# Kernel optimization log

Measured on AMD Instinct MI355X. Metric: run time of the kernel, lower is better.

The kernel has to match this reference:

```python
import jax, jax.numpy as jnp
import numpy as np

N, C, T, V = 64, 256, 120, 25
H, HD = 8, 32
DIM = H * HD  # 256, equals dim
K = 5        # number of joint groups
MAX_HOP = 5  # rpe rows = hops.max()+1


def conv1x1(w, x):
    # 1x1 Conv2d over [N, C, T, V]: pure channel mixing
    return jnp.einsum('oc,nctv->notv', w, x)


def setup_inputs() -> dict:
    key = jax.random.key(0)
    ks = jax.random.split(key, 10)
    s = 0.02
    return {
        'x': jax.random.normal(ks[0], (N, C, T, V), jnp.float32),
        'joint_label': jax.random.uniform(ks[1], (V, K), jnp.float32),
        'hops': jax.random.randint(ks[2], (V, V), 0, MAX_HOP, dtype=jnp.int32),
        'norm1_w': jnp.ones((C,), jnp.float32),
        'norm1_b': jnp.zeros((C,), jnp.float32),
        'q_w': jax.random.normal(ks[3], (DIM, C), jnp.float32) * s,
        'kv_w': jax.random.normal(ks[4], (2 * DIM, C), jnp.float32) * s,
        'proj_w': jax.random.normal(ks[5], (DIM, DIM), jnp.float32) * s,
        'proj_b': jnp.zeros((DIM,), jnp.float32),
        'rpe': jax.random.normal(ks[6], (MAX_HOP, DIM), jnp.float32) * s,
        'w1': jax.random.normal(ks[7], (H, HD), jnp.float32) * s,
        'outer': jnp.broadcast_to(jnp.eye(V, dtype=jnp.float32), (H, V, V)).copy(),
        'alpha': jnp.array([0.5], jnp.float32),
        'pe_w': jax.random.normal(ks[8], (DIM, C), jnp.float32) * s,
    }


def reference(x, joint_label, hops, norm1_w, norm1_b, q_w, kv_w,
              proj_w, proj_b, rpe, w1, outer, alpha, pe_w):
    n, c, t, v = x.shape
    h, hd = w1.shape
    dim = h * hd

    # ---- group embedding e (use_group, use_learned_partition == 'none') ----
    jl = joint_label  # [V, K]
    z = jnp.einsum('nctv,vk->nctk', x, jl / jl.sum(0, keepdims=True))
    z = jnp.einsum('dc,nctk->ndtk', pe_w, z)          # pe_proj (1x1 conv, no bias)
    e = jnp.einsum('ndtk,vk->ndtv', z, jl)            # z @ joint_label.T

    # ---- norm1: LayerNorm over channel dim ----
    mu = x.mean(axis=1, keepdims=True)
    var = x.var(axis=1, keepdims=True)
    xn = (x - mu) / jnp.sqrt(var + 1e-5)
    xn = xn * norm1_w[None, :, None, None] + norm1_b[None, :, None, None]

    # ---- q, k, v: 1x1 convs, reshape to [N, T, H, V, HD] ----
    def to_heads(y):
        return y.reshape(n, h, hd, t, v).transpose(0, 3, 1, 4, 2)

    q = to_heads(conv1x1(q_w, xn))
    k = to_heads(conv1x1(kv_w[:dim], xn))
    vv = to_heads(conv1x1(kv_w[dim:], xn))

    # ---- attention scores + biases ----
    attn = jnp.einsum('bthnc,bthmc->bthnm', q, k)
    # hop relative-position bias
    k_r = rpe[hops].reshape(v, v, h, hd)
    attn = attn + jnp.einsum('bthnc,nmhc->bthnm', q, k_r)
    # group embedding bias
    e_k = to_heads(e)
    attn = attn + jnp.einsum('bthnc,bthmc->bthnm', q, e_k)
    # group bias (broadcast over query dim)
    attn = attn + jnp.einsum('hc,bthmc->bthm', w1, e_k)[:, :, :, None, :]

    scale = hd ** (-0.5)
    attn = jax.nn.softmax(attn * scale, axis=-1)

    # ---- outer-blended attention @ v ----
    mix = alpha[0] * attn + outer[None, None]          # [N,T,H,V,V]
    o = jnp.einsum('bthnm,bthmc->bthnc', mix, vv)      # [N,T,H,V,HD]

    # back to [N, DIM, T, V]
    o = o.transpose(0, 1, 2, 4, 3).reshape(n, t, dim, v).transpose(0, 2, 1, 3)
    o = conv1x1(proj_w, o) + proj_b[None, :, None, None]

    # residual (dim_in == dim => plain skip)
    return x + o
```

## Files before the change

kernel.cpp:

```cpp
#include <hip/hip_runtime.h>


#define N_ 64
#define C_ 256
#define T_ 120
#define V_ 25
#define H_ 8
#define HD_ 32
#define K_ 5
#define TV_ 3000
#define CTV_ 768000

typedef unsigned short u16;
typedef __bf16 bf16x8 __attribute__((ext_vector_type(8)));
typedef float f32x4 __attribute__((ext_vector_type(4)));
typedef u16 u16x4 __attribute__((ext_vector_type(4)));

#define MFMA(a, b, c) __builtin_amdgcn_mfma_f32_16x16x32_bf16(a, b, c, 0, 0, 0)

__device__ __forceinline__ u16 bhi(float f) {
    union { float f; unsigned u; } c; c.f = f; return (u16)(c.u >> 16);
}
__device__ __forceinline__ float bhif(float f) {
    union { float f; unsigned u; } c; c.f = f; c.u &= 0xFFFF0000u; return c.f;
}

#define OFF_XT 0
#define XT_S 268
#define OFF_Z 6700
#define OFF_QB 7980
#define OFF_KB 15148
#define OFF_VB 22316
#define OFF_AT 29516
#define AT_S 27
#define OFF_QR 34916
#define OFF_BIAS 35916
#define OFF_MU 36116
#define OFF_RS 36141
#define OFF_INV 36166
#define OFF_JL 36171
#define OFF_W1 36296
#define OFF_HOPS 36552
#define SMEM_N 37177
#define OFF_PS OFF_VB
#define OFF_PSS (OFF_VB + 256)
#define OFF_Z2 (OFF_QB + 5120)
#define UZTH (OFF_QB * 2)
#define UZTL (OFF_QB * 2 + 4224)

#define WS_Q 0
#define WS_PE 393216
#define WS_PJ 524288

__global__ __launch_bounds__(256) void wprep(
    const float* __restrict__ qw, const float* __restrict__ kvw,
    const float* __restrict__ pew, const float* __restrict__ pjw,
    u16* __restrict__ ws)
{
    int fid = blockIdx.x * 256 + threadIdx.x;
    int seg, f;
    if (fid < 24576)      { seg = 0; f = fid; }
    else if (fid < 32768) { seg = 1; f = fid - 24576; }
    else                  { seg = 2; f = fid - 32768; }
    int mt = f >> 9, rem = f & 511, kt = rem >> 6, l = rem & 63;
    int row = mt * 16 + (l & 15);
    int k0 = kt * 32 + (l >> 4) * 8;
    const float* sp;
    u16* dp;
    if (seg == 0) {
        sp = (row < 256) ? (qw + row * 256 + k0) : (kvw + (row - 256) * 256 + k0);
        dp = ws + WS_Q + f * 16;
    } else if (seg == 1) {
        sp = pew + row * 256 + k0;
        dp = ws + WS_PE + f * 16;
    } else {
        sp = pjw + row * 256 + k0;
        dp = ws + WS_PJ + f * 16;
    }
    float4 a = *(const float4*)sp;
    float4 b = *(const float4*)(sp + 4);
    float w8[8] = {a.x, a.y, a.z, a.w, b.x, b.y, b.z, b.w};
    #pragma unroll
    for (int j = 0; j < 8; ++j) {
        float w = w8[j];
        dp[j] = bhi(w);
        dp[8 + j] = bhi(w - bhif(w));
    }
}

__global__ __launch_bounds__(512, 2) void fused_sttr(
    const float* __restrict__ x, const float* __restrict__ jl,
    const int* __restrict__ hops, const float* __restrict__ n1w,
    const float* __restrict__ n1b, const float* __restrict__ rpe,
    const float* __restrict__ pjb, const float* __restrict__ w1,
    const float* __restrict__ outer, const float* __restrict__ alpha,
    const u16* __restrict__ ws, float* __restrict__ out)
{
    __shared__ float sm[SMEM_N];
    u16* smu = reinterpret_cast<u16*>(sm);
    int* hopsS = (int*)(sm + OFF_HOPS);
    const int tid = threadIdx.x;
    const int bid = blockIdx.x;
    const int n = bid / T_;
    const int t = bid - n * T_;
    const int xbase = n * CTV_ + t * V_;
    const u16* wsq = ws + WS_Q;
    const u16* wspe = ws + WS_PE;
    const u16* wspj = ws + WS_PJ;
    const int wv = tid >> 6, ln = tid & 63;
    const int col = ln & 15, kg = ln >> 4;

    for (int i = tid; i < V_ * K_; i += 512) sm[OFF_JL + i] = jl[i];
    for (int i = tid; i < V_ * V_; i += 512) hopsS[i] = hops[i];
    for (int i = tid; i < H_ * HD_; i += 512) sm[OFF_W1 + i] = w1[i];
    for (int i = tid; i < C_ * V_; i += 512) {
        int c = i / V_, v = i - c * V_;
        sm[OFF_XT + v * XT_S + c] = x[xbase + c * TV_ + v];
    }
    __syncthreads();

    if (tid < K_) {
        float s = 0.f;
        for (int v = 0; v < V_; ++v) s += sm[OFF_JL + v * K_ + tid];
        sm[OFF_INV + tid] = 1.0f / s;
    } else if (tid >= 256 && tid < 456) {
        int i = tid - 256;
        int v = i % V_, p = i / V_;
        const float* row = &sm[OFF_XT + v * XT_S + p * 32];
        float s = 0.f, ss = 0.f;
        #pragma unroll
        for (int j = 0; j < 32; ++j) { float xx = row[j]; s += xx; ss += xx * xx; }
        sm[OFF_PS + p * 32 + v] = s;
        sm[OFF_PSS + p * 32 + v] = ss;
    }
    __syncthreads();

    if (tid < C_) {
        float a0 = 0, a1 = 0, a2 = 0, a3 = 0, a4 = 0;
        #pragma unroll
        for (int v = 0; v < V_; ++v) {
            float xv = sm[OFF_XT + v * XT_S + tid];
            const float* j5 = &sm[OFF_JL + v * K_];
            a0 += xv * j5[0]; a1 += xv * j5[1]; a2 += xv * j5[2];
            a3 += xv * j5[3]; a4 += xv * j5[4];
        }
        float* zr = &sm[OFF_Z + tid * K_];
        zr[0] = a0 * sm[OFF_INV + 0]; zr[1] = a1 * sm[OFF_INV + 1];
        zr[2] = a2 * sm[OFF_INV + 2]; zr[3] = a3 * sm[OFF_INV + 3];
        zr[4] = a4 * sm[OFF_INV + 4];
    } else if (tid < C_ + V_) {
        int v = tid - C_;
        float s = 0.f, ss = 0.f;
        #pragma unroll
        for (int p = 0; p < 8; ++p) { s += sm[OFF_PS + p * 32 + v]; ss += sm[OFF_PSS + p * 32 + v]; }
        float mu = s * (1.0f / 256.0f);
        float var = ss * (1.0f / 256.0f) - mu * mu;
        sm[OFF_MU + v] = mu;
        sm[OFF_RS + v] = rsqrtf(var + 1e-5f);
    }
    __syncthreads();

    float xr[32];
    {
        if (tid < 200) {
            int v = tid >> 3, cb = tid & 7, c0 = cb * 32;
            float mu = sm[OFF_MU + v], rs = sm[OFF_RS + v];
            #pragma unroll
            for (int j = 0; j < 32; ++j) {
                int c = c0 + j;
                xr[j] = (sm[OFF_XT + v * XT_S + c] - mu) * rs * n1w[c] + n1b[c];
            }
        } else if (tid >= 256) {
            int c = tid - 256;
            #pragma unroll
            for (int nn = 0; nn < K_; ++nn) {
                float f = sm[OFF_Z + c * K_ + nn];
                smu[UZTH + nn * 264 + c] = bhi(f);
                smu[UZTL + nn * 264 + c] = bhi(f - bhif(f));
            }
        }
    }
    __syncthreads();
    if (tid < 200) {
        int v = tid >> 3, cb = tid & 7, c0 = cb * 32;
        #pragma unroll
        for (int jb = 0; jb < 8; ++jb) {
            u16x4 hv, lv;
            #pragma unroll
            for (int j = 0; j < 4; ++j) {
                float f = xr[jb * 4 + j];
                hv[j] = bhi(f);
                lv[j] = bhi(f - bhif(f));
            }
            *(u16x4*)&smu[v * 536 + c0 + jb * 4] = hv;
            *(u16x4*)&smu[v * 536 + 256 + c0 + jb * 4] = lv;
        }
    }
    __syncthreads();

    {
        f32x4 zacc[2];
        #pragma unroll
        for (int i = 0; i < 2; ++i)
            #pragma unroll
            for (int r = 0; r < 4; ++r) zacc[i][r] = 0.f;
        for (int kt = 0; kt < 8; ++kt) {
            int bo = kt * 32 + kg * 8;
            bf16x8 zbh = *reinterpret_cast<const bf16x8*>(&smu[UZTH + col * 264 + bo]);
            bf16x8 zbl = *reinterpret_cast<const bf16x8*>(&smu[UZTL + col * 264 + bo]);
            #pragma unroll
            for (int i = 0; i < 2; ++i) {
                const u16* ap = wspe + (((wv * 2 + i) * 8 + kt) * 64 + ln) * 16;
                bf16x8 ah = *reinterpret_cast<const bf16x8*>(ap);
                bf16x8 al = *reinterpret_cast<const bf16x8*>(ap + 8);
                zacc[i] = MFMA(ah, zbh, zacc[i]);
                zacc[i] = MFMA(ah, zbl, zacc[i]);
                zacc[i] = MFMA(al, zbh, zacc[i]);
            }
        }
        if (col < K_) {
            #pragma unroll
            for (int i = 0; i < 2; ++i)
                #pragma unroll
                for (int r = 0; r < 4; ++r)
                    sm[OFF_Z2 + ((wv * 2 + i) * 16 + kg * 4 + r) * 8 + col] = zacc[i][r];
        }
    }
    __syncthreads();

    if (tid < C_) {
        float z0 = sm[OFF_Z2 + tid * 8 + 0], z1 = sm[OFF_Z2 + tid * 8 + 1];
        float z2_ = sm[OFF_Z2 + tid * 8 + 2], z3 = sm[OFF_Z2 + tid * 8 + 3];
        float z4 = sm[OFF_Z2 + tid * 8 + 4];
        float* kb = &sm[OFF_KB + tid * 28];
        #pragma unroll
        for (int v = 0; v < V_; ++v) {
            const float* j5 = &sm[OFF_JL + v * K_];
            kb[v] = z0 * j5[0] + z1 * j5[1] + z2_ * j5[2] + z3 * j5[3] + z4 * j5[4];
        }
    }
    __syncthreads();

    {
        f32x4 acc[6][2];
        #pragma unroll
        for (int i = 0; i < 6; ++i)
            #pragma unroll
            for (int nt = 0; nt < 2; ++nt)
                #pragma unroll
                for (int r = 0; r < 4; ++r) acc[i][nt][r] = 0.f;
        for (int kt = 0; kt < 8; ++kt) {
            int bo = kt * 32 + kg * 8;
            bf16x8 bh0 = *reinterpret_cast<const bf16x8*>(&smu[col * 536 + bo]);
            bf16x8 bl0 = *reinterpret_cast<const bf16x8*>(&smu[col * 536 + 256 + bo]);
            bf16x8 bh1 = *reinterpret_cast<const bf16x8*>(&smu[(col + 16) * 536 + bo]);
            bf16x8 bl1 = *reinterpret_cast<const bf16x8*>(&smu[(col + 16) * 536 + 256 + bo]);
            #pragma unroll
            for (int i = 0; i < 6; ++i) {
                const u16* ap = wsq + (((wv * 6 + i) * 8 + kt) * 64 + ln) * 16;
                bf16x8 ah = *reinterpret_cast<const bf16x8*>(ap);
                bf16x8 al = *reinterpret_cast<const bf16x8*>(ap + 8);
                acc[i][0] = MFMA(ah, bh0, acc[i][0]);
                acc[i][0] = MFMA(ah, bl0, acc[i][0]);
                acc[i][0] = MFMA(al, bh0, acc[i][0]);
                acc[i][1] = MFMA(ah, bh1, acc[i][1]);
                acc[i][1] = MFMA(ah, bl1, acc[i][1]);
                acc[i][1] = MFMA(al, bh1, acc[i][1]);
            }
        }
        if (tid < H_ * V_) {
            int h = tid / V_, m = tid - h * V_;
            float s = 0.f;
            #pragma unroll
            for (int c = 0; c < HD_; ++c)
                s += sm[OFF_W1 + h * HD_ + c] * sm[OFF_KB + (h * HD_ + c) * 28 + m];
            sm[OFF_BIAS + h * V_ + m] = s;
        }
        __syncthreads();
        #pragma unroll
        for (int i = 0; i < 6; ++i) {
            #pragma unroll
            for (int nt = 0; nt < 2; ++nt) {
                int v = nt * 16 + col;
                if (v < V_) {
                    #pragma unroll
                    for (int r = 0; r < 4; ++r) {
                        int row = (wv * 6 + i) * 16 + kg * 4 + r;
                        float val = acc[i][nt][r];
                        if (row < 256) sm[OFF_QB + row * 28 + v] = val;
                        else if (row < 512) sm[OFF_KB + (row - 256) * 28 + v] += val;
                        else {
                            int d = row - 512;
                            sm[OFF_VB + ((d >> 5) * V_ + v) * 36 + (d & 31)] = val;
                        }
                    }
                }
            }
        }
    }
    __syncthreads();

    for (int i = tid; i < H_ * V_ * K_; i += 512) {
        int h = i / (V_ * K_);
        int rem = i - h * (V_ * K_);
        int nq = rem / K_, hop = rem - nq * K_;
        const float* rp = rpe + hop * 256 + h * HD_;
        float s = 0.f;
        #pragma unroll
        for (int c = 0; c < HD_; ++c)
            s += sm[OFF_QB + (h * HD_ + c) * 28 + nq] * rp[c];
        sm[OFF_QR + (h * V_ + nq) * K_ + hop] = s;
    }
    __syncthreads();

    if (tid < 392) {
        int h = tid / 49;
        int r = tid - h * 49;
        int qg = r / 7, mg = r - qg * 7;
        int q0 = qg * 4, m0 = mg * 4;
        float acc[4][4];
        #pragma unroll
        for (int i = 0; i < 4; ++i)
            #pragma unroll
            for (int j = 0; j < 4; ++j) acc[i][j] = 0.f;
        for (int c = 0; c < HD_; ++c) {
            float4 q4 = *(const float4*)&sm[OFF_QB + (h * HD_ + c) * 28 + q0];
            float4 k4 = *(const float4*)&sm[OFF_KB + (h * HD_ + c) * 28 + m0];
            float qa[4] = {q4.x, q4.y, q4.z, q4.w};
            float ka[4] = {k4.x, k4.y, k4.z, k4.w};
            #pragma unroll
            for (int i = 0; i < 4; ++i)
                #pragma unroll
                for (int j = 0; j < 4; ++j) acc[i][j] += qa[i] * ka[j];
        }
        #pragma unroll
        for (int i = 0; i < 4; ++i) {
            int nq = q0 + i;
            if (nq < V_) {
                #pragma unroll
                for (int j = 0; j < 4; ++j) {
                    int m = m0 + j;
                    if (m < V_) {
                        int hop = hopsS[nq * V_ + m];
                        sm[OFF_AT + (h * V_ + nq) * AT_S + m] = acc[i][j]
                            + sm[OFF_QR + (h * V_ + nq) * K_ + hop]
                            + sm[OFF_BIAS + h * V_ + m];
                    }
                }
            }
        }
    }
    __syncthreads();

    if (tid < H_ * V_) {
        int h = tid / V_, nq = tid - h * V_;
        float* row = &sm[OFF_AT + (h * V_ + nq) * AT_S];
        const float sc = 0.17677669529663688f;
        float ev[25];
        float mx = -1e30f;
        #pragma unroll
        for (int j = 0; j < V_; ++j) { ev[j] = row[j] * sc; mx = fmaxf(mx, ev[j]); }
        float s = 0.f;
        #pragma unroll
        for (int j = 0; j < V_; ++j) { ev[j] = __expf(ev[j] - mx); s += ev[j]; }
        float inv = alpha[0] / s;
        const float* ob = outer + (h * V_ + nq) * V_;
        #pragma unroll
        for (int j = 0; j < V_; ++j) row[j] = ev[j] * inv + ob[j];
    }
    __syncthreads();

    if (tid < 320) {
        int h = tid / 40, r = tid % 40, ng = r >> 3, cg = r & 7;
        int n0 = ng * 5, c0 = cg * 4;
        float acc[5][4];
        #pragma unroll
        for (int i = 0; i < 5; ++i)
            #pragma unroll
            for (int j = 0; j < 4; ++j) acc[i][j] = 0.f;
        for (int m = 0; m < V_; ++m) {
            float4 vv = *(const float4*)&sm[OFF_VB + (h * V_ + m) * 36 + c0];
            #pragma unroll
            for (int i = 0; i < 5; ++i) {
                float mx = sm[OFF_AT + (h * V_ + n0 + i) * AT_S + m];
                acc[i][0] += mx * vv.x; acc[i][1] += mx * vv.y;
                acc[i][2] += mx * vv.z; acc[i][3] += mx * vv.w;
            }
        }
        int cb = h * HD_ + c0;
        #pragma unroll
        for (int i = 0; i < 5; ++i) {
            int row = n0 + i;
            u16x4 hv, lv;
            #pragma unroll
            for (int j = 0; j < 4; ++j) {
                float f = acc[i][j];
                hv[j] = bhi(f);
                lv[j] = bhi(f - bhif(f));
            }
            *(u16x4*)&smu[row * 536 + cb] = hv;
            *(u16x4*)&smu[row * 536 + 256 + cb] = lv;
        }
    }
    __syncthreads();

    {
        f32x4 pacc[2][2];
        #pragma unroll
        for (int i = 0; i < 2; ++i)
            #pragma unroll
            for (int nt = 0; nt < 2; ++nt)
                #pragma unroll
                for (int r = 0; r < 4; ++r) pacc[i][nt][r] = 0.f;
        for (int kt = 0; kt < 8; ++kt) {
            int bo = kt * 32 + kg * 8;
            bf16x8 oh0 = *reinterpret_cast<const bf16x8*>(&smu[col * 536 + bo]);
            bf16x8 ol0 = *reinterpret_cast<const bf16x8*>(&smu[col * 536 + 256 + bo]);
            bf16x8 oh1 = *reinterpret_cast<const bf16x8*>(&smu[(col + 16) * 536 + bo]);
            bf16x8 ol1 = *reinterpret_cast<const bf16x8*>(&smu[(col + 16) * 536 + 256 + bo]);
            #pragma unroll
            for (int i = 0; i < 2; ++i) {
                const u16* ap = wspj + (((wv * 2 + i) * 8 + kt) * 64 + ln) * 16;
                bf16x8 ah = *reinterpret_cast<const bf16x8*>(ap);
                bf16x8 al = *reinterpret_cast<const bf16x8*>(ap + 8);
                pacc[i][0] = MFMA(ah, oh0, pacc[i][0]);
                pacc[i][0] = MFMA(ah, ol0, pacc[i][0]);
                pacc[i][0] = MFMA(al, oh0, pacc[i][0]);
                pacc[i][1] = MFMA(ah, oh1, pacc[i][1]);
                pacc[i][1] = MFMA(ah, ol1, pacc[i][1]);
                pacc[i][1] = MFMA(al, oh1, pacc[i][1]);
            }
        }
        #pragma unroll
        for (int i = 0; i < 2; ++i) {
            #pragma unroll
            for (int nt = 0; nt < 2; ++nt) {
                int v = nt * 16 + col;
                if (v < V_) {
                    #pragma unroll
                    for (int r = 0; r < 4; ++r) {
                        int row = (wv * 2 + i) * 16 + kg * 4 + r;
                        int idx = xbase + row * TV_ + v;
                        out[idx] = pacc[i][nt][r] + pjb[row] + x[idx];
                    }
                }
            }
        }
    }
}

extern "C" void kernel_launch(void* const* d_in, const int* in_sizes, int n_in,
                              void* d_out, int out_size, void* d_ws, size_t ws_size,
                              hipStream_t stream) {
    const float* x     = (const float*)d_in[0];
    const float* jl    = (const float*)d_in[1];
    const int*   hops  = (const int*)  d_in[2];
    const float* n1w   = (const float*)d_in[3];
    const float* n1b   = (const float*)d_in[4];
    const float* qw    = (const float*)d_in[5];
    const float* kvw   = (const float*)d_in[6];
    const float* pjw   = (const float*)d_in[7];
    const float* pjb   = (const float*)d_in[8];
    const float* rpe   = (const float*)d_in[9];
    const float* w1    = (const float*)d_in[10];
    const float* outer = (const float*)d_in[11];
    const float* alpha = (const float*)d_in[12];
    const float* pew   = (const float*)d_in[13];
    u16* ws = (u16*)d_ws;

    wprep<<<160, 256, 0, stream>>>(qw, kvw, pew, pjw, ws);
    fused_sttr<<<N_ * T_, 512, 0, stream>>>(x, jl, hops, n1w, n1b, rpe, pjb,
                                            w1, outer, alpha, ws, (float*)d_out);
}
```

Before: 2.569 ms.

## Store activations as single bf16 in LDS, drop split-bf16 MFMAs, raise occupancy

Activations (normalized x, z, q, k, v, attention mix, attention output) are now kept in shared memory as single bf16 values instead of fp32 or split hi/lo bf16 pairs. This drops the third MFMA of each triple and roughly halves the LDS footprint. With the smaller footprint the launch bound asks for 4 blocks per CU instead of 2, so more blocks can be resident. The trade-off is lower accuracy, since activations are rounded to bf16 while only the weights keep their hi/lo split.

New measurement: 2.763 ms. 1.08x slower.

```diff
diff --git a/kernel.cpp b/kernel.cpp
--- a/kernel.cpp
+++ b/kernel.cpp
@@ -24,29 +24,29 @@
 __device__ __forceinline__ float bhif(float f) {
     union { float f; unsigned u; } c; c.f = f; c.u &= 0xFFFF0000u; return c.f;
 }
-
-#define OFF_XT 0
-#define XT_S 268
-#define OFF_Z 6700
-#define OFF_QB 7980
-#define OFF_KB 15148
-#define OFF_VB 22316
-#define OFF_AT 29516
-#define AT_S 27
-#define OFF_QR 34916
-#define OFF_BIAS 35916
-#define OFF_MU 36116
-#define OFF_RS 36141
-#define OFF_INV 36166
-#define OFF_JL 36171
-#define OFF_W1 36296
-#define OFF_HOPS 36552
-#define SMEM_N 37177
-#define OFF_PS OFF_VB
-#define OFF_PSS (OFF_VB + 256)
-#define OFF_Z2 (OFF_QB + 5120)
-#define UZTH (OFF_QB * 2)
-#define UZTL (OFF_QB * 2 + 4224)
+__device__ __forceinline__ float b2f(u16 u) {
+    union { unsigned u; float f; } c; c.u = ((unsigned)u) << 16; return c.f;
+}
+
+#define U_XT 0
+#define U_Q 0
+#define U_O 0
+#define U_Z2 7168
+#define U_QR 11264
+#define U_XN 13264
+#define U_AT 13264
+#define U_ZT 19864
+#define U_K 19864
+#define U_PS 27032
+#define U_V 27032
+#define U_JL 34232
+#define U_INV 34482
+#define U_W1 34492
+#define U_MU 35004
+#define U_RS 35054
+#define U_BIAS 35104
+#define U_HOPS 35504
+#define SMEM_U 36768
 
 #define WS_Q 0
 #define WS_PE 393216
@@ -88,7 +88,7 @@
     }
 }
 
-__global__ __launch_bounds__(512, 2) void fused_sttr(
+__global__ __launch_bounds__(512, 4) void fused_sttr(
     const float* __restrict__ x, const float* __restrict__ jl,
     const int* __restrict__ hops, const float* __restrict__ n1w,
     const float* __restrict__ n1b, const float* __restrict__ rpe,
@@ -96,42 +96,52 @@
     const float* __restrict__ outer, const float* __restrict__ alpha,
     const u16* __restrict__ ws, float* __restrict__ out)
 {
-    __shared__ float sm[SMEM_N];
-    u16* smu = reinterpret_cast<u16*>(sm);
-    int* hopsS = (int*)(sm + OFF_HOPS);
+    __shared__ u16 smu[SMEM_U];
+    float* xTf   = (float*)smu;
+    float* Z2f   = (float*)(smu + U_Z2);
+    float* QRf   = (float*)(smu + U_QR);
+    float* PSf   = (float*)(smu + U_PS);
+    float* JLf   = (float*)(smu + U_JL);
+    float* INVf  = (float*)(smu + U_INV);
+    float* W1f   = (float*)(smu + U_W1);
+    float* MUf   = (float*)(smu + U_MU);
+    float* RSf   = (float*)(smu + U_RS);
+    float* BIASf = (float*)(smu + U_BIAS);
+    int* hopsS   = (int*)(smu + U_HOPS);
+
     const int tid = threadIdx.x;
     const int bid = blockIdx.x;
     const int n = bid / T_;
     const int t = bid - n * T_;
     const int xbase = n * CTV_ + t * V_;
-    const u16* wsq = ws + WS_Q;
+    const u16* wsq  = ws + WS_Q;
     const u16* wspe = ws + WS_PE;
     const u16* wspj = ws + WS_PJ;
     const int wv = tid >> 6, ln = tid & 63;
     const int col = ln & 15, kg = ln >> 4;
 
-    for (int i = tid; i < V_ * K_; i += 512) sm[OFF_JL + i] = jl[i];
+    for (int i = tid; i < V_ * K_; i += 512) JLf[i] = jl[i];
     for (int i = tid; i < V_ * V_; i += 512) hopsS[i] = hops[i];
-    for (int i = tid; i < H_ * HD_; i += 512) sm[OFF_W1 + i] = w1[i];
+    for (int i = tid; i < H_ * HD_; i += 512) W1f[i] = w1[i];
     for (int i = tid; i < C_ * V_; i += 512) {
         int c = i / V_, v = i - c * V_;
-        sm[OFF_XT + v * XT_S + c] = x[xbase + c * TV_ + v];
+        xTf[v * 264 + c] = x[xbase + c * TV_ + v];
     }
     __syncthreads();
 
     if (tid < K_) {
         float s = 0.f;
-        for (int v = 0; v < V_; ++v) s += sm[OFF_JL + v * K_ + tid];
-        sm[OFF_INV + tid] = 1.0f / s;
+        for (int v = 0; v < V_; ++v) s += JLf[v * K_ + tid];
+        INVf[tid] = 1.0f / s;
     } else if (tid >= 256 && tid < 456) {
         int i = tid - 256;
-        int v = i % V_, p = i / V_;
-        const float* row = &sm[OFF_XT + v * XT_S + p * 32];
+        int v = i % 25, p = i / 25;
+        const float* row = &xTf[v * 264 + p * 32];
         float s = 0.f, ss = 0.f;
         #pragma unroll
         for (int j = 0; j < 32; ++j) { float xx = row[j]; s += xx; ss += xx * xx; }
-        sm[OFF_PS + p * 32 + v] = s;
-        sm[OFF_PSS + p * 32 + v] = ss;
+        PSf[p * 32 + v] = s;
+        PSf[256 + p * 32 + v] = ss;
     }
     __syncthreads();
 
@@ -139,61 +149,35 @@
         float a0 = 0, a1 = 0, a2 = 0, a3 = 0, a4 = 0;
         #pragma unroll
         for (int v = 0; v < V_; ++v) {
-            float xv = sm[OFF_XT + v * XT_S + tid];
-            const float* j5 = &sm[OFF_JL + v * K_];
+            float xv = xTf[v * 264 + tid];
+            const float* j5 = &JLf[v * K_];
             a0 += xv * j5[0]; a1 += xv * j5[1]; a2 += xv * j5[2];
             a3 += xv * j5[3]; a4 += xv * j5[4];
         }
-        float* zr = &sm[OFF_Z + tid * K_];
-        zr[0] = a0 * sm[OFF_INV + 0]; zr[1] = a1 * sm[OFF_INV + 1];
-        zr[2] = a2 * sm[OFF_INV + 2]; zr[3] = a3 * sm[OFF_INV + 3];
-        zr[4] = a4 * sm[OFF_INV + 4];
+        smu[U_ZT + 0 * 264 + tid] = bhi(a0 * INVf[0]);
+        smu[U_ZT + 1 * 264 + tid] = bhi(a1 * INVf[1]);
+        smu[U_ZT + 2 * 264 + tid] = bhi(a2 * INVf[2]);
+        smu[U_ZT + 3 * 264 + tid] = bhi(a3 * INVf[3]);
+        smu[U_ZT + 4 * 264 + tid] = bhi(a4 * INVf[4]);
     } else if (tid < C_ + V_) {
         int v = tid - C_;
         float s = 0.f, ss = 0.f;
         #pragma unroll
-        for (int p = 0; p < 8; ++p) { s += sm[OFF_PS + p * 32 + v]; ss += sm[OFF_PSS + p * 32 + v]; }
+        for (int p = 0; p < 8; ++p) { s += PSf[p * 32 + v]; ss += PSf[256 + p * 32 + v]; }
         float mu = s * (1.0f / 256.0f);
         float var = ss * (1.0f / 256.0f) - mu * mu;
-        sm[OFF_MU + v] = mu;
-        sm[OFF_RS + v] = rsqrtf(var + 1e-5f);
-    }
-    __syncthreads();
-
-    float xr[32];
+        MUf[v] = mu;
+        RSf[v] = rsqrtf(var + 1e-5f);
+    }
+    __syncthreads();
+
     {
-        if (tid < 200) {
-            int v = tid >> 3, cb = tid & 7, c0 = cb * 32;
-            float mu = sm[OFF_MU + v], rs = sm[OFF_RS + v];
-            #pragma unroll
-            for (int j = 0; j < 32; ++j) {
-                int c = c0 + j;
-                xr[j] = (sm[OFF_XT + v * XT_S + c] - mu) * rs * n1w[c] + n1b[c];
-            }
-        } else if (tid >= 256) {
-            int c = tid - 256;
-            #pragma unroll
-            for (int nn = 0; nn < K_; ++nn) {
-                float f = sm[OFF_Z + c * K_ + nn];
-                smu[UZTH + nn * 264 + c] = bhi(f);
-                smu[UZTL + nn * 264 + c] = bhi(f - bhif(f));
-            }
-        }
-    }
-    __syncthreads();
-    if (tid < 200) {
-        int v = tid >> 3, cb = tid & 7, c0 = cb * 32;
-        #pragma unroll
-        for (int jb = 0; jb < 8; ++jb) {
-            u16x4 hv, lv;
-            #pragma unroll
-            for (int j = 0; j < 4; ++j) {
-                float f = xr[jb * 4 + j];
-                hv[j] = bhi(f);
-                lv[j] = bhi(f - bhif(f));
-            }
-            *(u16x4*)&smu[v * 536 + c0 + jb * 4] = hv;
-            *(u16x4*)&smu[v * 536 + 256 + c0 + jb * 4] = lv;
+        int c = tid & 255, half = tid >> 8;
+        int v0 = half ? 12 : 0, v1 = half ? 25 : 12;
+        float w = n1w[c], b = n1b[c];
+        for (int v = v0; v < v1; ++v) {
+            float xv = xTf[v * 264 + c];
+            smu[U_XN + v * 264 + c] = bhi((xv - MUf[v]) * RSf[v] * w + b);
         }
     }
     __syncthreads();
@@ -206,16 +190,14 @@
             for (int r = 0; r < 4; ++r) zacc[i][r] = 0.f;
         for (int kt = 0; kt < 8; ++kt) {
             int bo = kt * 32 + kg * 8;
-            bf16x8 zbh = *reinterpret_cast<const bf16x8*>(&smu[UZTH + col * 264 + bo]);
-            bf16x8 zbl = *reinterpret_cast<const bf16x8*>(&smu[UZTL + col * 264 + bo]);
+            bf16x8 zb = *reinterpret_cast<const bf16x8*>(&smu[U_ZT + col * 264 + bo]);
             #pragma unroll
             for (int i = 0; i < 2; ++i) {
                 const u16* ap = wspe + (((wv * 2 + i) * 8 + kt) * 64 + ln) * 16;
                 bf16x8 ah = *reinterpret_cast<const bf16x8*>(ap);
                 bf16x8 al = *reinterpret_cast<const bf16x8*>(ap + 8);
-                zacc[i] = MFMA(ah, zbh, zacc[i]);
-                zacc[i] = MFMA(ah, zbl, zacc[i]);
-                zacc[i] = MFMA(al, zbh, zacc[i]);
+                zacc[i] = MFMA(ah, zb, zacc[i]);
+                zacc[i] = MFMA(al, zb, zacc[i]);
             }
         }
         if (col < K_) {
@@ -223,20 +205,20 @@
             for (int i = 0; i < 2; ++i)
                 #pragma unroll
                 for (int r = 0; r < 4; ++r)
-                    sm[OFF_Z2 + ((wv * 2 + i) * 16 + kg * 4 + r) * 8 + col] = zacc[i][r];
-        }
-    }
-    __syncthreads();
-
-    if (tid < C_) {
-        float z0 = sm[OFF_Z2 + tid * 8 + 0], z1 = sm[OFF_Z2 + tid * 8 + 1];
-        float z2_ = sm[OFF_Z2 + tid * 8 + 2], z3 = sm[OFF_Z2 + tid * 8 + 3];
-        float z4 = sm[OFF_Z2 + tid * 8 + 4];
-        float* kb = &sm[OFF_KB + tid * 28];
-        #pragma unroll
-        for (int v = 0; v < V_; ++v) {
-            const float* j5 = &sm[OFF_JL + v * K_];
-            kb[v] = z0 * j5[0] + z1 * j5[1] + z2_ * j5[2] + z3 * j5[3] + z4 * j5[4];
+                    Z2f[((wv * 2 + i) * 16 + kg * 4 + r) * 8 + col] = zacc[i][r];
+        }
+    }
+    __syncthreads();
+
+    {
+        int c = tid & 255, half = tid >> 8;
+        int v0 = half ? 12 : 0, v1 = half ? 25 : 12;
+        float z0 = Z2f[c * 8 + 0], z1 = Z2f[c * 8 + 1], z2 = Z2f[c * 8 + 2];
+        float z3 = Z2f[c * 8 + 3], z4 = Z2f[c * 8 + 4];
+        for (int v = v0; v < v1; ++v) {
+            const float* j5 = &JLf[v * K_];
+            float e = z0 * j5[0] + z1 * j5[1] + z2 * j5[2] + z3 * j5[3] + z4 * j5[4];
+            smu[U_K + c * 28 + v] = bhi(e);
         }
     }
     __syncthreads();
@@ -251,21 +233,17 @@
                 for (int r = 0; r < 4; ++r) acc[i][nt][r] = 0.f;
         for (int kt = 0; kt < 8; ++kt) {
             int bo = kt * 32 + kg * 8;
-            bf16x8 bh0 = *reinterpret_cast<const bf16x8*>(&smu[col * 536 + bo]);
-            bf16x8 bl0 = *reinterpret_cast<const bf16x8*>(&smu[col * 536 + 256 + bo]);
-            bf16x8 bh1 = *reinterpret_cast<const bf16x8*>(&smu[(col + 16) * 536 + bo]);
-            bf16x8 bl1 = *reinterpret_cast<const bf16x8*>(&smu[(col + 16) * 536 + 256 + bo]);
+            bf16x8 b0 = *reinterpret_cast<const bf16x8*>(&smu[U_XN + col * 264 + bo]);
+            bf16x8 b1 = *reinterpret_cast<const bf16x8*>(&smu[U_XN + (col + 16) * 264 + bo]);
             #pragma unroll
             for (int i = 0; i < 6; ++i) {
                 const u16* ap = wsq + (((wv * 6 + i) * 8 + kt) * 64 + ln) * 16;
                 bf16x8 ah = *reinterpret_cast<const bf16x8*>(ap);
                 bf16x8 al = *reinterpret_cast<const bf16x8*>(ap + 8);
-                acc[i][0] = MFMA(ah, bh0, acc[i][0]);
-                acc[i][0] = MFMA(ah, bl0, acc[i][0]);
-                acc[i][0] = MFMA(al, bh0, acc[i][0]);
-                acc[i][1] = MFMA(ah, bh1, acc[i][1]);
-                acc[i][1] = MFMA(ah, bl1, acc[i][1]);
-                acc[i][1] = MFMA(al, bh1, acc[i][1]);
+                acc[i][0] = MFMA(ah, b0, acc[i][0]);
+                acc[i][0] = MFMA(al, b0, acc[i][0]);
+                acc[i][1] = MFMA(ah, b1, acc[i][1]);
+                acc[i][1] = MFMA(al, b1, acc[i][1]);
             }
         }
         if (tid < H_ * V_) {
@@ -273,8 +251,8 @@
             float s = 0.f;
             #pragma unroll
             for (int c = 0; c < HD_; ++c)
-                s += sm[OFF_W1 + h * HD_ + c] * sm[OFF_KB + (h * HD_ + c) * 28 + m];
-            sm[OFF_BIAS + h * V_ + m] = s;
+                s += W1f[h * HD_ + c] * b2f(smu[U_K + (h * HD_ + c) * 28 + m]);
+            BIASf[tid] = s;
         }
         __syncthreads();
         #pragma unroll
@@ -287,11 +265,14 @@
                     for (int r = 0; r < 4; ++r) {
                         int row = (wv * 6 + i) * 16 + kg * 4 + r;
                         float val = acc[i][nt][r];
-                        if (row < 256) sm[OFF_QB + row * 28 + v] = val;
-                        else if (row < 512) sm[OFF_KB + (row - 256) * 28 + v] += val;
-                        else {
+                        if (row < 256) {
+                            smu[U_Q + row * 28 + v] = bhi(val);
+                        } else if (row < 512) {
+                            int a = U_K + (row - 256) * 28 + v;
+                            smu[a] = bhi(b2f(smu[a]) + val);
+                        } else {
                             int d = row - 512;
-                            sm[OFF_VB + ((d >> 5) * V_ + v) * 36 + (d & 31)] = val;
+                            smu[U_V + ((d >> 5) * V_ + v) * 36 + (d & 31)] = bhi(val);
                         }
                     }
                 }
@@ -308,8 +289,8 @@
         float s = 0.f;
         #pragma unroll
         for (int c = 0; c < HD_; ++c)
-            s += sm[OFF_QB + (h * HD_ + c) * 28 + nq] * rp[c];
-        sm[OFF_QR + (h * V_ + nq) * K_ + hop] = s;
+            s += b2f(smu[U_Q + (h * HD_ + c) * 28 + nq]) * rp[c];
+        QRf[(h * V_ + nq) * K_ + hop] = s;
     }
     __syncthreads();
 
@@ -324,10 +305,10 @@
             #pragma unroll
             for (int j = 0; j < 4; ++j) acc[i][j] = 0.f;
         for (int c = 0; c < HD_; ++c) {
-            float4 q4 = *(const float4*)&sm[OFF_QB + (h * HD_ + c) * 28 + q0];
-            float4 k4 = *(const float4*)&sm[OFF_KB + (h * HD_ + c) * 28 + m0];
-            float qa[4] = {q4.x, q4.y, q4.z, q4.w};
-            float ka[4] = {k4.x, k4.y, k4.z, k4.w};
+            u16x4 q4 = *(const u16x4*)&smu[U_Q + (h * HD_ + c) * 28 + q0];
+            u16x4 k4 = *(const u16x4*)&smu[U_K + (h * HD_ + c) * 28 + m0];
+            float qa[4] = {b2f(q4[0]), b2f(q4[1]), b2f(q4[2]), b2f(q4[3])};
+            float ka[4] = {b2f(k4[0]), b2f(k4[1]), b2f(k4[2]), b2f(k4[3])};
             #pragma unroll
             for (int i = 0; i < 4; ++i)
                 #pragma unroll
@@ -342,9 +323,9 @@
                     int m = m0 + j;
                     if (m < V_) {
                         int hop = hopsS[nq * V_ + m];
-                        sm[OFF_AT + (h * V_ + nq) * AT_S + m] = acc[i][j]
-                            + sm[OFF_QR + (h * V_ + nq) * K_ + hop]
-                            + sm[OFF_BIAS + h * V_ + m];
+                        float val = acc[i][j] + QRf[(h * V_ + nq) * K_ + hop]
+                                  + BIASf[h * V_ + m];
+                        smu[U_AT + (h * V_ + nq) * 28 + m] = bhi(val);
                     }
                 }
             }
@@ -354,19 +335,19 @@
 
     if (tid < H_ * V_) {
         int h = tid / V_, nq = tid - h * V_;
-        float* row = &sm[OFF_AT + (h * V_ + nq) * AT_S];
+        u16* row = &smu[U_AT + (h * V_ + nq) * 28];
         const float sc = 0.17677669529663688f;
         float ev[25];
         float mx = -1e30f;
         #pragma unroll
-        for (int j = 0; j < V_; ++j) { ev[j] = row[j] * sc; mx = fmaxf(mx, ev[j]); }
+        for (int j = 0; j < V_; ++j) { ev[j] = b2f(row[j]) * sc; mx = fmaxf(mx, ev[j]); }
         float s = 0.f;
         #pragma unroll
         for (int j = 0; j < V_; ++j) { ev[j] = __expf(ev[j] - mx); s += ev[j]; }
         float inv = alpha[0] / s;
         const float* ob = outer + (h * V_ + nq) * V_;
         #pragma unroll
-        for (int j = 0; j < V_; ++j) row[j] = ev[j] * inv + ob[j];
+        for (int j = 0; j < V_; ++j) row[j] = bhi(ev[j] * inv + ob[j]);
     }
     __syncthreads();
 
@@ -379,27 +360,22 @@
             #pragma unroll
             for (int j = 0; j < 4; ++j) acc[i][j] = 0.f;
         for (int m = 0; m < V_; ++m) {
-            float4 vv = *(const float4*)&sm[OFF_VB + (h * V_ + m) * 36 + c0];
+            u16x4 v4 = *(const u16x4*)&smu[U_V + (h * V_ + m) * 36 + c0];
+            float va[4] = {b2f(v4[0]), b2f(v4[1]), b2f(v4[2]), b2f(v4[3])};
             #pragma unroll
             for (int i = 0; i < 5; ++i) {
-                float mx = sm[OFF_AT + (h * V_ + n0 + i) * AT_S + m];
-                acc[i][0] += mx * vv.x; acc[i][1] += mx * vv.y;
-                acc[i][2] += mx * vv.z; acc[i][3] += mx * vv.w;
+                float mixv = b2f(smu[U_AT + (h * V_ + n0 + i) * 28 + m]);
+                acc[i][0] += mixv * va[0]; acc[i][1] += mixv * va[1];
+                acc[i][2] += mixv * va[2]; acc[i][3] += mixv * va[3];
             }
         }
         int cb = h * HD_ + c0;
         #pragma unroll
         for (int i = 0; i < 5; ++i) {
-            int row = n0 + i;
-            u16x4 hv, lv;
-            #pragma unroll
-            for (int j = 0; j < 4; ++j) {
-                float f = acc[i][j];
-                hv[j] = bhi(f);
-                lv[j] = bhi(f - bhif(f));
-            }
-            *(u16x4*)&smu[row * 536 + cb] = hv;
-            *(u16x4*)&smu[row * 536 + 256 + cb] = lv;
+            u16x4 w4;
+            #pragma unroll
+            for (int j = 0; j < 4; ++j) w4[j] = bhi(acc[i][j]);
+            *(u16x4*)&smu[U_O + (n0 + i) * 264 + cb] = w4;
         }
     }
     __syncthreads();
@@ -414,21 +390,17 @@
                 for (int r = 0; r < 4; ++r) pacc[i][nt][r] = 0.f;
         for (int kt = 0; kt < 8; ++kt) {
             int bo = kt * 32 + kg * 8;
-            bf16x8 oh0 = *reinterpret_cast<const bf16x8*>(&smu[col * 536 + bo]);
-            bf16x8 ol0 = *reinterpret_cast<const bf16x8*>(&smu[col * 536 + 256 + bo]);
-            bf16x8 oh1 = *reinterpret_cast<const bf16x8*>(&smu[(col + 16) * 536 + bo]);
-            bf16x8 ol1 = *reinterpret_cast<const bf16x8*>(&smu[(col + 16) * 536 + 256 + bo]);
+            bf16x8 o0 = *reinterpret_cast<const bf16x8*>(&smu[U_O + col * 264 + bo]);
+            bf16x8 o1 = *reinterpret_cast<const bf16x8*>(&smu[U_O + (col + 16) * 264 + bo]);
             #pragma unroll
             for (int i = 0; i < 2; ++i) {
                 const u16* ap = wspj + (((wv * 2 + i) * 8 + kt) * 64 + ln) * 16;
                 bf16x8 ah = *reinterpret_cast<const bf16x8*>(ap);
                 bf16x8 al = *reinterpret_cast<const bf16x8*>(ap + 8);
-                pacc[i][0] = MFMA(ah, oh0, pacc[i][0]);
-                pacc[i][0] = MFMA(ah, ol0, pacc[i][0]);
-                pacc[i][0] = MFMA(al, oh0, pacc[i][0]);
-                pacc[i][1] = MFMA(ah, oh1, pacc[i][1]);
-                pacc[i][1] = MFMA(ah, ol1, pacc[i][1]);
-                pacc[i][1] = MFMA(al, oh1, pacc[i][1]);
+                pacc[i][0] = MFMA(ah, o0, pacc[i][0]);
+                pacc[i][0] = MFMA(al, o0, pacc[i][0]);
+                pacc[i][1] = MFMA(ah, o1, pacc[i][1]);
+                pacc[i][1] = MFMA(al, o1, pacc[i][1]);
             }
         }
         #pragma unroll
```
